# Optimization experiments

Measured on AMD Instinct MI355X. Metric: run time of the kernel, lower is better.

The kernel has to match this reference:

```python
import jax, jax.numpy as jnp
import numpy as np

B, N, D, F, H, C, L = 64, 8192, 5, 16, 4, 4, 4
NEG_SLOPE = 0.2


def setup_inputs() -> dict:
    key = jax.random.key(0)
    ks = jax.random.split(key, 16)
    lin = lambda k, fi, fo: (jax.random.normal(k, (fi, fo), jnp.float32) / np.sqrt(fi)).astype(jnp.float32)
    x = jax.random.normal(ks[0], (B, N, F), jnp.float32)
    agent_nodes = jax.random.randint(ks[1], (B,), 0, N, dtype=jnp.int32)
    neighbors = jax.random.randint(ks[2], (N, D), 0, N, dtype=jnp.int32)
    # GATv2 params (L layers, all 16 -> 4 heads x 4 = 16)
    Wl = jax.random.normal(ks[3], (L, F, H, C), jnp.float32) / np.sqrt(F)
    Wr = jax.random.normal(ks[4], (L, F, H, C), jnp.float32) / np.sqrt(F)
    att_w = jax.random.normal(ks[5], (L, H, C), jnp.float32) / np.sqrt(C)
    bias = jnp.zeros((L, H * C), jnp.float32)
    # global classifier 16->32->64, edge classifier 99->16->8->1
    Wg1, bg1 = lin(ks[6], H * C, 2 * H * C), jnp.zeros(2 * H * C, jnp.float32)
    Wg2, bg2 = lin(ks[7], 2 * H * C, 4 * H * C), jnp.zeros(4 * H * C, jnp.float32)
    e_in = 2 * H * C + 3 + 4 * H * C  # 99
    We1, be1 = lin(ks[8], e_in, H * C), jnp.zeros(H * C, jnp.float32)
    We2, be2 = lin(ks[9], H * C, H * C // 2), jnp.zeros(H * C // 2, jnp.float32)
    We3, be3 = lin(ks[10], H * C // 2, 1), jnp.zeros(1, jnp.float32)
    return dict(x=x, agent_nodes=agent_nodes, neighbors=neighbors, Wl=Wl, Wr=Wr,
                att_w=att_w, bias=bias, Wg1=Wg1, bg1=bg1, Wg2=Wg2, bg2=bg2,
                We1=We1, be1=be1, We2=We2, be2=be2, We3=We3, be3=be3)


def _gatv2_layer(h, src, dst, wl, wr, a, b, n_nodes):
    # h: [B,N,Fin]; wl/wr: [Fin,H,C]; a: [H,C]; b: [H*C]
    xl = jnp.einsum('bnf,fhc->bnhc', h, wl)   # source transform
    xr = jnp.einsum('bnf,fhc->bnhc', h, wr)   # target transform
    hs = xl[:, src]                            # [B,E,H,C]
    ht = xr[:, dst]
    logit = jnp.einsum('behc,hc->beh', jax.nn.leaky_relu(hs + ht, NEG_SLOPE), a)
    lt = logit.transpose(1, 0, 2)              # [E,B,H] (segment ops need E first)
    m = jax.ops.segment_max(lt, dst, num_segments=n_nodes)
    w = jnp.exp(lt - m[dst])
    s = jax.ops.segment_sum(w, dst, num_segments=n_nodes)
    alpha = w / (s[dst] + 1e-16)               # [E,B,H] softmax over in-edges of dst
    msg = alpha[..., None] * hs.transpose(1, 0, 2, 3)
    out = jax.ops.segment_sum(msg, dst, num_segments=n_nodes)  # [N,B,H,C]
    return out.transpose(1, 0, 2, 3).reshape(h.shape[0], n_nodes, -1) + b


def reference(x, agent_nodes, neighbors, Wl, Wr, att_w, bias,
              Wg1, bg1, Wg2, bg2, We1, be1, We2, be2, We3, be3):
    Bn, Nn, _ = x.shape
    Dd = neighbors.shape[1]
    loop = jnp.arange(Nn, dtype=neighbors.dtype)
    src = jnp.concatenate([jnp.repeat(loop, Dd), loop])   # add_self_loops
    dst = jnp.concatenate([neighbors.reshape(-1), loop])
    h = x
    for i in range(Wl.shape[0]):
        h = _gatv2_layer(h, src, dst, Wl[i], Wr[i], att_w[i], bias[i], Nn)
    # global mean aggregation -> 2 SlimFC(tanh)
    agg = jnp.tanh(h.mean(axis=1) @ Wg1 + bg1)
    agg = jnp.tanh(agg @ Wg2 + bg2)                        # [B,64]
    # agent out-edges: source node + its D neighbors
    nb = neighbors[agent_nodes]                            # [B,D]
    bi = jnp.arange(Bn)
    source = h[bi, agent_nodes]                            # [B,16]
    target = h[bi[:, None], nb]                            # [B,D,16]
    tok = jnp.eye(3, dtype=h.dtype)                        # 3 one-hot act tokens
    feats = jnp.concatenate([
        jnp.broadcast_to(source[:, None, None, :], (Bn, 3, Dd, source.shape[-1])),
        jnp.broadcast_to(tok[None, :, None, :], (Bn, 3, Dd, 3)),
        jnp.broadcast_to(target[:, None, :, :], (Bn, 3, Dd, target.shape[-1])),
        jnp.broadcast_to(agg[:, None, None, :], (Bn, 3, Dd, agg.shape[-1])),
    ], axis=-1)                                            # [B,3,D,99]
    e = jnp.tanh(feats @ We1 + be1)
    e = jnp.tanh(e @ We2 + be2)
    e = (e @ We3 + be3)[..., 0]                            # [B,3,D]
    # logits[b, turn*D + move] (convert_multidiscrete_action_to_discrete)
    return e.reshape(Bn, 3 * Dd)
```

## Files before the change

kernel.cpp:

```cpp
#include <hip/hip_runtime.h>
#include <hip/hip_fp16.h>
#include <cmath>

#define NNODES 8192
#define NB 64
#define ND 5
#define MAXDEG 64
#define NBLK_T0 2048
#define NBLK_LAY 8192



__global__ void __launch_bounds__(256)
k_t0fill(const float* __restrict__ x, const float* __restrict__ Wl0, const float* __restrict__ Wr0,
         __half* __restrict__ xl0, __half* __restrict__ xr0,
         const int* __restrict__ agent, const int* __restrict__ nbr,
         int* __restrict__ cnt, int* __restrict__ slot, int* __restrict__ needed) {
  if (blockIdx.x >= NBLK_T0) {
    int eb = blockIdx.x - NBLK_T0;
    if (eb < 160) {
      int i = eb*256 + threadIdx.x;
      int v = nbr[i];
      int pos = atomicAdd(&cnt[v], 1);
      slot[v*MAXDEG + 1 + pos] = i/ND;
    } else if (threadIdx.x < NB) {
      int an = agent[threadIdx.x];
      needed[an] = 1;
      #pragma unroll
      for (int d = 0; d < ND; ++d) needed[nbr[an*ND + d]] = 1;
    }
    return;
  }
  int gid = blockIdx.x*blockDim.x + threadIdx.x;
  int n = gid >> 6;
  int b = gid & 63;
  const float4* src = (const float4*)(x + (((size_t)b*NNODES + n) << 4));
  float hv[16];
  #pragma unroll
  for (int q = 0; q < 4; ++q) *(float4*)(hv+4*q) = src[q];
  float yl[16], yr[16];
  #pragma unroll
  for (int j = 0; j < 16; ++j) { yl[j] = 0.f; yr[j] = 0.f; }
  #pragma unroll
  for (int f = 0; f < 16; ++f) {
    float hf = hv[f];
    #pragma unroll
    for (int j = 0; j < 16; ++j) {
      yl[j] = fmaf(hf, Wl0[f*16+j], yl[j]);
      yr[j] = fmaf(hf, Wr0[f*16+j], yr[j]);
    }
  }
  size_t idx = ((size_t)n << 10) + (b << 4);
  __half2 lh[8], rh[8];
  #pragma unroll
  for (int j = 0; j < 8; ++j) {
    lh[j] = __floats2half2_rn(yl[2*j], yl[2*j+1]);
    rh[j] = __floats2half2_rn(yr[2*j], yr[2*j+1]);
  }
  float4* ld = (float4*)(xl0 + idx);
  ld[0] = *(float4*)&lh[0]; ld[1] = *(float4*)&lh[4];
  float4* rd = (float4*)(xr0 + idx);
  rd[0] = *(float4*)&rh[0]; rd[1] = *(float4*)&rh[4];
}


template<bool LAST>
__global__ void __launch_bounds__(256)
k_layer(const __half* __restrict__ xlin, const __half* __restrict__ xrin,
        __half* __restrict__ xlout, __half* __restrict__ xrout,
        const float* __restrict__ WlNext, const float* __restrict__ WrNext,
        const float* __restrict__ att, const float* __restrict__ bias,
        const int* __restrict__ cnt, const int* __restrict__ slot,
        const int* __restrict__ needed, __half* __restrict__ h,
        float* __restrict__ meanpart) {
  __shared__ float sW[544];
  __shared__ float msm[4][16][17];
  int tid = threadIdx.x;
  int w = tid >> 6, lane = tid & 63;

  if (!LAST) {
    sW[tid]     = WlNext[tid];
    sW[256+tid] = WrNext[tid];
  }
  if (tid < 16)      sW[512+tid]    = att[tid];
  else if (tid < 32) sW[512+tid]    = bias[tid-16];
  __syncthreads();

  int wv = (blockIdx.x << 2) + w;
  int q = wv >> 13;
  int v = wv & (NNODES-1);
  int head = lane & 3;
  size_t soff = ((size_t)q << 8) + (lane << 2);

  float4 awv = *(float4*)&sW[512 + head*4];
  float aw0 = awv.x, aw1 = awv.y, aw2 = awv.z, aw3 = awv.w;

  float xr0, xr1, xr2, xr3;
  {
    float2 rx = *(const float2*)(xrin + (((size_t)v) << 10) + soff);
    __half2* ph = (__half2*)&rx;
    float2 f0 = __half22float2(ph[0]), f1 = __half22float2(ph[1]);
    xr0 = f0.x; xr1 = f0.y; xr2 = f1.x; xr3 = f1.y;
  }

  float s = 0.f, a0 = 0.f, a1 = 0.f, a2 = 0.f, a3 = 0.f;
  int deg = cnt[v];
  int tot = deg + 1;
  const int* sl = slot + v*MAXDEG;

  auto loadrow = [&](int u) -> float2 {
    return *(const float2*)(xlin + (((size_t)u) << 10) + soff);
  };
  auto process = [&](float2 r) {
    __half2* ph = (__half2*)&r;
    float2 f0 = __half22float2(ph[0]), f1 = __half22float2(ph[1]);
    float t0 = f0.x, t1 = f0.y, t2 = f1.x, t3 = f1.y;
    float z0 = t0 + xr0; z0 = (z0 >= 0.f) ? z0 : 0.2f*z0;
    float z1 = t1 + xr1; z1 = (z1 >= 0.f) ? z1 : 0.2f*z1;
    float z2 = t2 + xr2; z2 = (z2 >= 0.f) ? z2 : 0.2f*z2;
    float z3 = t3 + xr3; z3 = (z3 >= 0.f) ? z3 : 0.2f*z3;
    float lg = fmaf(z0, aw0, fmaf(z1, aw1, fmaf(z2, aw2, z3*aw3)));
    float p = __expf(lg);
    s += p;
    a0 = fmaf(p, t0, a0); a1 = fmaf(p, t1, a1);
    a2 = fmaf(p, t2, a2); a3 = fmaf(p, t3, a3);
  };

  float2 r0, r1, r2, r3, r4, r5, r6, r7, pA, pB;
  r0 = loadrow(v);
  if (tot > 1) r1 = loadrow(sl[1]);
  if (tot > 2) r2 = loadrow(sl[2]);
  if (tot > 3) r3 = loadrow(sl[3]);
  if (tot > 4) r4 = loadrow(sl[4]);
  if (tot > 5) r5 = loadrow(sl[5]);
  if (tot > 6) r6 = loadrow(sl[6]);
  if (tot > 7) r7 = loadrow(sl[7]);
  if (tot > 8) pA = loadrow(sl[8]);
  if (tot > 9) pB = loadrow(sl[9]);
  process(r0);
  if (tot > 1) process(r1);
  if (tot > 2) process(r2);
  if (tot > 3) process(r3);
  if (tot > 4) process(r4);
  if (tot > 5) process(r5);
  if (tot > 6) process(r6);
  if (tot > 7) process(r7);
  int e = 8;
  for (; e+1 < tot; e += 2) {
    float2 cA = pA; if (e+2 < tot) pA = loadrow(sl[e+2]);
    float2 cB = pB; if (e+3 < tot) pB = loadrow(sl[e+3]);
    process(cA); process(cB);
  }
  if (e < tot) process(pA);

  float inv = 1.f / s;
  float4 bsv = *(float4*)&sW[528 + head*4];
  float o0 = fmaf(a0, inv, bsv.x), o1 = fmaf(a1, inv, bsv.y);
  float o2 = fmaf(a2, inv, bsv.z), o3 = fmaf(a3, inv, bsv.w);

  if (!LAST) {
    float of[16];
    int lb = lane & ~3;
    #pragma unroll
    for (int src = 0; src < 4; ++src) {
      of[src*4+0] = __shfl(o0, lb+src);
      of[src*4+1] = __shfl(o1, lb+src);
      of[src*4+2] = __shfl(o2, lb+src);
      of[src*4+3] = __shfl(o3, lb+src);
    }
    float yl0=0.f, yl1=0.f, yl2=0.f, yl3=0.f;
    float yr0=0.f, yr1=0.f, yr2=0.f, yr3=0.f;
    #pragma unroll
    for (int f = 0; f < 16; ++f) {
      float4 wl4 = *(float4*)&sW[f*16 + head*4];
      float4 wr4 = *(float4*)&sW[256 + f*16 + head*4];
      float ofv = of[f];
      yl0 = fmaf(ofv, wl4.x, yl0); yl1 = fmaf(ofv, wl4.y, yl1);
      yl2 = fmaf(ofv, wl4.z, yl2); yl3 = fmaf(ofv, wl4.w, yl3);
      yr0 = fmaf(ofv, wr4.x, yr0); yr1 = fmaf(ofv, wr4.y, yr1);
      yr2 = fmaf(ofv, wr4.z, yr2); yr3 = fmaf(ofv, wr4.w, yr3);
    }
    float2 lo, ro;
    ((__half2*)&lo)[0] = __floats2half2_rn(yl0, yl1);
    ((__half2*)&lo)[1] = __floats2half2_rn(yl2, yl3);
    ((__half2*)&ro)[0] = __floats2half2_rn(yr0, yr1);
    ((__half2*)&ro)[1] = __floats2half2_rn(yr2, yr3);
    size_t idx = (((size_t)v) << 10) + soff;
    *(float2*)(xlout + idx) = lo;
    *(float2*)(xrout + idx) = ro;
  } else {
    if (needed[v]) {
      float2 ho;
      ((__half2*)&ho)[0] = __floats2half2_rn(o0, o1);
      ((__half2*)&ho)[1] = __floats2half2_rn(o2, o3);
      *(float2*)(h + (((size_t)v) << 10) + soff) = ho;
    }
    int bl = lane >> 2;
    msm[w][bl][head*4+0] = o0;
    msm[w][bl][head*4+1] = o1;
    msm[w][bl][head*4+2] = o2;
    msm[w][bl][head*4+3] = o3;
    __syncthreads();
    int bl2 = tid >> 4, hc = tid & 15;
    float ssum = msm[0][bl2][hc] + msm[1][bl2][hc] + msm[2][bl2][hc] + msm[3][bl2][hc];
    meanpart[(size_t)blockIdx.x*256 + tid] = ssum;
  }
}


__global__ void __launch_bounds__(256)
k_tail(const __half* __restrict__ h, const int* __restrict__ agent,
       const int* __restrict__ nbr, const float* __restrict__ meanpart,
       const float* __restrict__ Wg1, const float* __restrict__ bg1,
       const float* __restrict__ Wg2, const float* __restrict__ bg2,
       const float* __restrict__ We1, const float* __restrict__ be1,
       const float* __restrict__ We2, const float* __restrict__ be2,
       const float* __restrict__ We3, const float* __restrict__ be3,
       float* __restrict__ out) {
  int b = blockIdx.x;
  int t = threadIdx.x;
  __shared__ float red[256];
  __shared__ float mean[16], g1[32], aggs[64];
  __shared__ float srcv[16];
  __shared__ float tgt[5][16];
  __shared__ float e1s[15][16];
  __shared__ float e2s[15][8];
  int an = agent[b];

  {
    int hc = t & 15, grp = t >> 4;
    int q = b >> 4, bl = b & 15;
    float s = 0.f;
    int base = q*2048 + grp*128;
    for (int p = 0; p < 128; ++p)
      s += meanpart[(size_t)(base+p)*256 + bl*16 + hc];
    red[t] = s;
    __syncthreads();
    if (t < 16) {
      float m = 0.f;
      for (int g = 0; g < 16; ++g) m += red[g*16 + t];
      mean[t] = m * (1.0f/NNODES);
    }
  }
  if (t >= 64 && t < 80) srcv[t-64] = __half2float(h[((size_t)an << 10) + (b << 4) + (t-64)]);
  if (t >= 96 && t < 176) {
    int d = (t-96)/16, k = (t-96)%16;
    int nn = nbr[an*ND + d];
    tgt[d][k] = __half2float(h[((size_t)nn << 10) + (b << 4) + k]);
  }
  __syncthreads();
  if (t < 32) {
    float a = bg1[t];
    for (int f = 0; f < 16; ++f) a = fmaf(mean[f], Wg1[f*32+t], a);
    g1[t] = tanhf(a);
  }
  __syncthreads();
  if (t < 64) {
    float a = bg2[t];
    for (int f = 0; f < 32; ++f) a = fmaf(g1[f], Wg2[f*64+t], a);
    aggs[t] = tanhf(a);
  }
  __syncthreads();
  if (t < 240) {
    int j = t & 15, td = t >> 4;
    int tk = td/5, d = td%5;
    float a = be1[j];
    for (int k = 0; k < 16; ++k) a = fmaf(srcv[k],  We1[k*16+j],      a);
    a += We1[(16+tk)*16 + j];
    for (int k = 0; k < 16; ++k) a = fmaf(tgt[d][k], We1[(19+k)*16+j], a);
    for (int k = 0; k < 64; ++k) a = fmaf(aggs[k],  We1[(35+k)*16+j], a);
    e1s[td][j] = tanhf(a);
  }
  __syncthreads();
  if (t < 120) {
    int j = t & 7, td = t >> 3;
    float a = be2[j];
    for (int k = 0; k < 16; ++k) a = fmaf(e1s[td][k], We2[k*8+j], a);
    e2s[td][j] = tanhf(a);
  }
  __syncthreads();
  if (t < 15) {
    float a = be3[0];
    for (int k = 0; k < 8; ++k) a = fmaf(e2s[t][k], We3[k], a);
    out[b*15 + t] = a;
  }
}


extern "C" void kernel_launch(void* const* d_in, const int* in_sizes, int n_in,
                              void* d_out, int out_size, void* d_ws, size_t ws_size,
                              hipStream_t stream) {
  const float* x     = (const float*)d_in[0];
  const int*   agent = (const int*)  d_in[1];
  const int*   nbr   = (const int*)  d_in[2];
  const float* Wl    = (const float*)d_in[3];
  const float* Wr    = (const float*)d_in[4];
  const float* att   = (const float*)d_in[5];
  const float* bias  = (const float*)d_in[6];
  const float* Wg1   = (const float*)d_in[7];
  const float* bg1   = (const float*)d_in[8];
  const float* Wg2   = (const float*)d_in[9];
  const float* bg2   = (const float*)d_in[10];
  const float* We1   = (const float*)d_in[11];
  const float* be1   = (const float*)d_in[12];
  const float* We2   = (const float*)d_in[13];
  const float* be2   = (const float*)d_in[14];
  const float* We3   = (const float*)d_in[15];
  const float* be3   = (const float*)d_in[16];
  float* out = (float*)d_out;

  char* ws = (char*)d_ws;
  size_t off = 0;
  auto alloc = [&](size_t bytes) -> void* {
    void* p = ws + off;
    off += (bytes + 255) & ~(size_t)255;
    return p;
  };
  const size_t XBYTES = (size_t)NNODES*NB*16*sizeof(__half);
  __half* h    = (__half*)alloc(XBYTES);
  __half* xlA  = (__half*)alloc(XBYTES);
  __half* xlB  = (__half*)alloc(XBYTES);
  __half* xrA  = (__half*)alloc(XBYTES);
  __half* xrB  = (__half*)alloc(XBYTES);
  int*  slot   = (int*)alloc((size_t)NNODES*MAXDEG*sizeof(int));
  float* meanpart = (float*)alloc((size_t)NBLK_LAY*256*sizeof(float));
  int* cnt    = (int*)alloc(NNODES*sizeof(int));
  int* needed = (int*)alloc(NNODES*sizeof(int));

  hipMemsetAsync(cnt, 0, NNODES*sizeof(int)*2, stream);

  k_t0fill<<<NBLK_T0 + 161, 256, 0, stream>>>(x, Wl, Wr, xlA, xrA,
                                              agent, nbr, cnt, slot, needed);

  k_layer<false><<<NBLK_LAY, 256, 0, stream>>>(xlA, xrA, xlB, xrB, Wl + 256, Wr + 256,
                                               att,      bias,      cnt, slot, needed, nullptr, nullptr);
  k_layer<false><<<NBLK_LAY, 256, 0, stream>>>(xlB, xrB, xlA, xrA, Wl + 512, Wr + 512,
                                               att + 16, bias + 16, cnt, slot, needed, nullptr, nullptr);
  k_layer<false><<<NBLK_LAY, 256, 0, stream>>>(xlA, xrA, xlB, xrB, Wl + 768, Wr + 768,
                                               att + 32, bias + 32, cnt, slot, needed, nullptr, nullptr);
  k_layer<true ><<<NBLK_LAY, 256, 0, stream>>>(xlB, xrB, nullptr, nullptr, nullptr, nullptr,
                                               att + 48, bias + 48, cnt, slot, needed, h, meanpart);

  k_tail<<<NB, 256, 0, stream>>>(h, agent, nbr, meanpart,
                                 Wg1, bg1, Wg2, bg2,
                                 We1, be1, We2, be2, We3, be3, out);
}
```

Baseline: 239.1 us.

## Map one lane per batch element with all heads per lane in GAT layers

Each wavefront now handles one node across all 64 batch elements, with each lane computing all 4 heads over 16 features, instead of four wavefronts per node splitting the batch into quarters with one head per lane. This removes the cross-lane shuffles for the next-layer projection, widens loads to two float4 per row, and cuts the block count by four. It also reshapes the meanpart reduction layout and the tail's read of it. The cost is higher register pressure (16 accumulators plus 32 projection outputs per lane), a shallower neighbour prefetch, and a larger shared-memory buffer for the mean reduction.

```diff
diff --git a/kernel.cpp b/kernel.cpp
--- a/kernel.cpp
+++ b/kernel.cpp
@@ -7,7 +7,7 @@
 #define ND 5
 #define MAXDEG 64
 #define NBLK_T0 2048
-#define NBLK_LAY 8192
+#define NBLK_LAY 2048
 
 
 
@@ -64,6 +64,8 @@
 }
 
 
+struct Row { float4 c0, c1; };
+
 template<bool LAST>
 __global__ void __launch_bounds__(256)
 k_layer(const __half* __restrict__ xlin, const __half* __restrict__ xrin,
@@ -74,7 +76,6 @@
         const int* __restrict__ needed, __half* __restrict__ h,
         float* __restrict__ meanpart) {
   __shared__ float sW[544];
-  __shared__ float msm[4][16][17];
   int tid = threadIdx.x;
   int w = tid >> 6, lane = tid & 63;
 
@@ -86,124 +87,148 @@
   else if (tid < 32) sW[512+tid]    = bias[tid-16];
   __syncthreads();
 
-  int wv = (blockIdx.x << 2) + w;
-  int q = wv >> 13;
-  int v = wv & (NNODES-1);
-  int head = lane & 3;
-  size_t soff = ((size_t)q << 8) + (lane << 2);
-
-  float4 awv = *(float4*)&sW[512 + head*4];
-  float aw0 = awv.x, aw1 = awv.y, aw2 = awv.z, aw3 = awv.w;
-
-  float xr0, xr1, xr2, xr3;
+  int v = (blockIdx.x << 2) + w;
+  size_t loff = (size_t)(lane << 4);
+
+  float aw[16];
+  #pragma unroll
+  for (int k = 0; k < 16; ++k) aw[k] = sW[512+k];
+
+  float xrf[16];
   {
-    float2 rx = *(const float2*)(xrin + (((size_t)v) << 10) + soff);
-    __half2* ph = (__half2*)&rx;
-    float2 f0 = __half22float2(ph[0]), f1 = __half22float2(ph[1]);
-    xr0 = f0.x; xr1 = f0.y; xr2 = f1.x; xr3 = f1.y;
-  }
-
-  float s = 0.f, a0 = 0.f, a1 = 0.f, a2 = 0.f, a3 = 0.f;
+    const float4* p = (const float4*)(xrin + (((size_t)v) << 10) + loff);
+    float4 c0 = p[0], c1 = p[1];
+    __half2* ph0 = (__half2*)&c0;
+    __half2* ph1 = (__half2*)&c1;
+    #pragma unroll
+    for (int j = 0; j < 4; ++j) {
+      float2 f0 = __half22float2(ph0[j]);
+      xrf[2*j]   = f0.x; xrf[2*j+1]   = f0.y;
+      float2 f1 = __half22float2(ph1[j]);
+      xrf[8+2*j] = f1.x; xrf[8+2*j+1] = f1.y;
+    }
+  }
+
+  float s4[4] = {0.f, 0.f, 0.f, 0.f};
+  float a[16];
+  #pragma unroll
+  for (int k = 0; k < 16; ++k) a[k] = 0.f;
+
   int deg = cnt[v];
   int tot = deg + 1;
   const int* sl = slot + v*MAXDEG;
 
-  auto loadrow = [&](int u) -> float2 {
-    return *(const float2*)(xlin + (((size_t)u) << 10) + soff);
+  auto loadrow = [&](int u) -> Row {
+    const float4* p = (const float4*)(xlin + (((size_t)u) << 10) + loff);
+    Row r; r.c0 = p[0]; r.c1 = p[1]; return r;
   };
-  auto process = [&](float2 r) {
-    __half2* ph = (__half2*)&r;
-    float2 f0 = __half22float2(ph[0]), f1 = __half22float2(ph[1]);
-    float t0 = f0.x, t1 = f0.y, t2 = f1.x, t3 = f1.y;
-    float z0 = t0 + xr0; z0 = (z0 >= 0.f) ? z0 : 0.2f*z0;
-    float z1 = t1 + xr1; z1 = (z1 >= 0.f) ? z1 : 0.2f*z1;
-    float z2 = t2 + xr2; z2 = (z2 >= 0.f) ? z2 : 0.2f*z2;
-    float z3 = t3 + xr3; z3 = (z3 >= 0.f) ? z3 : 0.2f*z3;
-    float lg = fmaf(z0, aw0, fmaf(z1, aw1, fmaf(z2, aw2, z3*aw3)));
-    float p = __expf(lg);
-    s += p;
-    a0 = fmaf(p, t0, a0); a1 = fmaf(p, t1, a1);
-    a2 = fmaf(p, t2, a2); a3 = fmaf(p, t3, a3);
+  auto process = [&](Row r) {
+    float t[16];
+    __half2* ph0 = (__half2*)&r.c0;
+    __half2* ph1 = (__half2*)&r.c1;
+    #pragma unroll
+    for (int j = 0; j < 4; ++j) {
+      float2 f0 = __half22float2(ph0[j]);
+      t[2*j]   = f0.x; t[2*j+1]   = f0.y;
+      float2 f1 = __half22float2(ph1[j]);
+      t[8+2*j] = f1.x; t[8+2*j+1] = f1.y;
+    }
+    #pragma unroll
+    for (int hd = 0; hd < 4; ++hd) {
+      float z0 = t[4*hd+0] + xrf[4*hd+0]; z0 = (z0 >= 0.f) ? z0 : 0.2f*z0;
+      float z1 = t[4*hd+1] + xrf[4*hd+1]; z1 = (z1 >= 0.f) ? z1 : 0.2f*z1;
+      float z2 = t[4*hd+2] + xrf[4*hd+2]; z2 = (z2 >= 0.f) ? z2 : 0.2f*z2;
+      float z3 = t[4*hd+3] + xrf[4*hd+3]; z3 = (z3 >= 0.f) ? z3 : 0.2f*z3;
+      float lg = fmaf(z0, aw[4*hd+0], fmaf(z1, aw[4*hd+1],
+                 fmaf(z2, aw[4*hd+2], z3*aw[4*hd+3])));
+      float p = __expf(lg);
+      s4[hd] += p;
+      a[4*hd+0] = fmaf(p, t[4*hd+0], a[4*hd+0]);
+      a[4*hd+1] = fmaf(p, t[4*hd+1], a[4*hd+1]);
+      a[4*hd+2] = fmaf(p, t[4*hd+2], a[4*hd+2]);
+      a[4*hd+3] = fmaf(p, t[4*hd+3], a[4*hd+3]);
+    }
   };
 
-  float2 r0, r1, r2, r3, r4, r5, r6, r7, pA, pB;
+  Row r0, r1, r2, r3, pA, pB;
   r0 = loadrow(v);
   if (tot > 1) r1 = loadrow(sl[1]);
   if (tot > 2) r2 = loadrow(sl[2]);
   if (tot > 3) r3 = loadrow(sl[3]);
-  if (tot > 4) r4 = loadrow(sl[4]);
-  if (tot > 5) r5 = loadrow(sl[5]);
-  if (tot > 6) r6 = loadrow(sl[6]);
-  if (tot > 7) r7 = loadrow(sl[7]);
-  if (tot > 8) pA = loadrow(sl[8]);
-  if (tot > 9) pB = loadrow(sl[9]);
+  if (tot > 4) pA = loadrow(sl[4]);
+  if (tot > 5) pB = loadrow(sl[5]);
   process(r0);
   if (tot > 1) process(r1);
   if (tot > 2) process(r2);
   if (tot > 3) process(r3);
-  if (tot > 4) process(r4);
-  if (tot > 5) process(r5);
-  if (tot > 6) process(r6);
-  if (tot > 7) process(r7);
-  int e = 8;
+  int e = 4;
   for (; e+1 < tot; e += 2) {
-    float2 cA = pA; if (e+2 < tot) pA = loadrow(sl[e+2]);
-    float2 cB = pB; if (e+3 < tot) pB = loadrow(sl[e+3]);
+    Row cA = pA; if (e+2 < tot) pA = loadrow(sl[e+2]);
+    Row cB = pB; if (e+3 < tot) pB = loadrow(sl[e+3]);
     process(cA); process(cB);
   }
   if (e < tot) process(pA);
 
-  float inv = 1.f / s;
-  float4 bsv = *(float4*)&sW[528 + head*4];
-  float o0 = fmaf(a0, inv, bsv.x), o1 = fmaf(a1, inv, bsv.y);
-  float o2 = fmaf(a2, inv, bsv.z), o3 = fmaf(a3, inv, bsv.w);
+  float o[16];
+  #pragma unroll
+  for (int hd = 0; hd < 4; ++hd) {
+    float inv = 1.f / s4[hd];
+    #pragma unroll
+    for (int k = 0; k < 4; ++k)
+      o[4*hd+k] = fmaf(a[4*hd+k], inv, sW[528+4*hd+k]);
+  }
 
   if (!LAST) {
-    float of[16];
-    int lb = lane & ~3;
-    #pragma unroll
-    for (int src = 0; src < 4; ++src) {
-      of[src*4+0] = __shfl(o0, lb+src);
-      of[src*4+1] = __shfl(o1, lb+src);
-      of[src*4+2] = __shfl(o2, lb+src);
-      of[src*4+3] = __shfl(o3, lb+src);
-    }
-    float yl0=0.f, yl1=0.f, yl2=0.f, yl3=0.f;
-    float yr0=0.f, yr1=0.f, yr2=0.f, yr3=0.f;
+    float yl[16], yr[16];
+    #pragma unroll
+    for (int j = 0; j < 16; ++j) { yl[j] = 0.f; yr[j] = 0.f; }
     #pragma unroll
     for (int f = 0; f < 16; ++f) {
-      float4 wl4 = *(float4*)&sW[f*16 + head*4];
-      float4 wr4 = *(float4*)&sW[256 + f*16 + head*4];
-      float ofv = of[f];
-      yl0 = fmaf(ofv, wl4.x, yl0); yl1 = fmaf(ofv, wl4.y, yl1);
-      yl2 = fmaf(ofv, wl4.z, yl2); yl3 = fmaf(ofv, wl4.w, yl3);
-      yr0 = fmaf(ofv, wr4.x, yr0); yr1 = fmaf(ofv, wr4.y, yr1);
-      yr2 = fmaf(ofv, wr4.z, yr2); yr3 = fmaf(ofv, wr4.w, yr3);
-    }
-    float2 lo, ro;
-    ((__half2*)&lo)[0] = __floats2half2_rn(yl0, yl1);
-    ((__half2*)&lo)[1] = __floats2half2_rn(yl2, yl3);
-    ((__half2*)&ro)[0] = __floats2half2_rn(yr0, yr1);
-    ((__half2*)&ro)[1] = __floats2half2_rn(yr2, yr3);
-    size_t idx = (((size_t)v) << 10) + soff;
-    *(float2*)(xlout + idx) = lo;
-    *(float2*)(xrout + idx) = ro;
+      float ofv = o[f];
+      #pragma unroll
+      for (int j4 = 0; j4 < 4; ++j4) {
+        float4 wl4 = *(float4*)&sW[f*16 + j4*4];
+        float4 wr4 = *(float4*)&sW[256 + f*16 + j4*4];
+        yl[j4*4+0] = fmaf(ofv, wl4.x, yl[j4*4+0]);
+        yl[j4*4+1] = fmaf(ofv, wl4.y, yl[j4*4+1]);
+        yl[j4*4+2] = fmaf(ofv, wl4.z, yl[j4*4+2]);
+        yl[j4*4+3] = fmaf(ofv, wl4.w, yl[j4*4+3]);
+        yr[j4*4+0] = fmaf(ofv, wr4.x, yr[j4*4+0]);
+        yr[j4*4+1] = fmaf(ofv, wr4.y, yr[j4*4+1]);
+        yr[j4*4+2] = fmaf(ofv, wr4.z, yr[j4*4+2]);
+        yr[j4*4+3] = fmaf(ofv, wr4.w, yr[j4*4+3]);
+      }
+    }
+    __half2 lh[8], rh[8];
+    #pragma unroll
+    for (int j = 0; j < 8; ++j) {
+      lh[j] = __floats2half2_rn(yl[2*j], yl[2*j+1]);
+      rh[j] = __floats2half2_rn(yr[2*j], yr[2*j+1]);
+    }
+    size_t idx = (((size_t)v) << 10) + loff;
+    float4* ld = (float4*)(xlout + idx);
+    ld[0] = *(float4*)&lh[0]; ld[1] = *(float4*)&lh[4];
+    float4* rd = (float4*)(xrout + idx);
+    rd[0] = *(float4*)&rh[0]; rd[1] = *(float4*)&rh[4];
   } else {
     if (needed[v]) {
-      float2 ho;
-      ((__half2*)&ho)[0] = __floats2half2_rn(o0, o1);
-      ((__half2*)&ho)[1] = __floats2half2_rn(o2, o3);
-      *(float2*)(h + (((size_t)v) << 10) + soff) = ho;
-    }
-    int bl = lane >> 2;
-    msm[w][bl][head*4+0] = o0;
-    msm[w][bl][head*4+1] = o1;
-    msm[w][bl][head*4+2] = o2;
-    msm[w][bl][head*4+3] = o3;
+      __half2 hh[8];
+      #pragma unroll
+      for (int j = 0; j < 8; ++j) hh[j] = __floats2half2_rn(o[2*j], o[2*j+1]);
+      float4* hd = (float4*)(h + (((size_t)v) << 10) + loff);
+      hd[0] = *(float4*)&hh[0]; hd[1] = *(float4*)&hh[4];
+    }
+    __shared__ float msm[4][16][64];
+    #pragma unroll
+    for (int k = 0; k < 16; ++k) msm[w][k][lane] = o[k];
     __syncthreads();
-    int bl2 = tid >> 4, hc = tid & 15;
-    float ssum = msm[0][bl2][hc] + msm[1][bl2][hc] + msm[2][bl2][hc] + msm[3][bl2][hc];
-    meanpart[(size_t)blockIdx.x*256 + tid] = ssum;
+    #pragma unroll
+    for (int c = 0; c < 4; ++c) {
+      int hc = c*4 + w;
+      int b  = lane;
+      float ssum = msm[0][hc][b] + msm[1][hc][b] + msm[2][hc][b] + msm[3][hc][b];
+      meanpart[(size_t)blockIdx.x*1024 + hc*64 + b] = ssum;
+    }
   }
 }
 
@@ -229,11 +254,10 @@
 
   {
     int hc = t & 15, grp = t >> 4;
-    int q = b >> 4, bl = b & 15;
     float s = 0.f;
-    int base = q*2048 + grp*128;
+    int base = grp*128;
     for (int p = 0; p < 128; ++p)
-      s += meanpart[(size_t)(base+p)*256 + bl*16 + hc];
+      s += meanpart[(size_t)(base+p)*1024 + hc*64 + b];
     red[t] = s;
     __syncthreads();
     if (t < 16) {
@@ -323,7 +347,7 @@
   __half* xrA  = (__half*)alloc(XBYTES);
   __half* xrB  = (__half*)alloc(XBYTES);
   int*  slot   = (int*)alloc((size_t)NNODES*MAXDEG*sizeof(int));
-  float* meanpart = (float*)alloc((size_t)NBLK_LAY*256*sizeof(float));
+  float* meanpart = (float*)alloc((size_t)NBLK_LAY*1024*sizeof(float));
   int* cnt    = (int*)alloc(NNODES*sizeof(int));
   int* needed = (int*)alloc(NNODES*sizeof(int));
 
```

After: 274.5 us. 14.8% more time.
